# Performance work log

Measured on AMD Instinct MI355X. Metric: run time of the kernel, lower is better.

The kernel has to match this reference:

```python
import jax, jax.numpy as jnp
import numpy as np

LUT_DIM = 33
CTX_DIM = 128


def _identity_lut(dim):
    coords = jnp.linspace(0.0, 1.0, dim)
    r, g, b = jnp.meshgrid(coords, coords, coords, indexing='ij')
    return jnp.stack([r, g, b], axis=-1)  # [dim, dim, dim, 3], axes (r,g,b)


def setup_inputs() -> dict:
    key = jax.random.key(0)
    ks = jax.random.split(key, 8)
    B, H, W = 4, 512, 512
    image = jax.random.normal(ks[0], (B, 3, H, W), dtype=jnp.float32)
    spatial_context = jax.random.normal(ks[1], (B, CTX_DIM, H, W), dtype=jnp.float32)
    s = 0.05
    params = {
        'base_lut': _identity_lut(LUT_DIM),
        'W1': jax.random.normal(ks[2], (128, CTX_DIM), dtype=jnp.float32) * s,
        'b1': jnp.zeros((128,), dtype=jnp.float32),
        'W2': jax.random.normal(ks[3], (64, 128), dtype=jnp.float32) * s,
        'b2': jnp.zeros((64,), dtype=jnp.float32),
        'W3': jax.random.normal(ks[4], (3, 64), dtype=jnp.float32) * s,
        'b3': jnp.zeros((3,), dtype=jnp.float32),
        'offset_scale': jnp.float32(0.1),
    }
    return {'image': image, 'spatial_context': spatial_context, **params}


def _conv1x1(x, W, b):
    # x: [B,Cin,H,W], W: [Cout,Cin]
    return jnp.einsum('bchw,oc->bohw', x, W) + b[None, :, None, None]


def _trilinear_lut(lut_flat, gx, gy, gz, dim):
    # lut_flat: [3, dim^3] (flattened over z,y,x = r,g,b axes)
    # gx,gy,gz: [B,H,W] float coords in [0, dim-1]; border padding via clamp
    fmax = jnp.float32(dim - 1)
    gx = jnp.clip(gx, 0.0, fmax)
    gy = jnp.clip(gy, 0.0, fmax)
    gz = jnp.clip(gz, 0.0, fmax)
    x0 = jnp.floor(gx).astype(jnp.int32)
    y0 = jnp.floor(gy).astype(jnp.int32)
    z0 = jnp.floor(gz).astype(jnp.int32)
    x1 = jnp.minimum(x0 + 1, dim - 1)
    y1 = jnp.minimum(y0 + 1, dim - 1)
    z1 = jnp.minimum(z0 + 1, dim - 1)
    fx = gx - x0.astype(gx.dtype)
    fy = gy - y0.astype(gy.dtype)
    fz = gz - z0.astype(gz.dtype)

    def gather(zi, yi, xi):
        idx = (zi * dim + yi) * dim + xi  # [B,H,W]
        return lut_flat[:, idx]  # [3,B,H,W]

    c000 = gather(z0, y0, x0); c001 = gather(z0, y0, x1)
    c010 = gather(z0, y1, x0); c011 = gather(z0, y1, x1)
    c100 = gather(z1, y0, x0); c101 = gather(z1, y0, x1)
    c110 = gather(z1, y1, x0); c111 = gather(z1, y1, x1)

    fx = fx[None]; fy = fy[None]; fz = fz[None]
    c00 = c000 * (1 - fx) + c001 * fx
    c01 = c010 * (1 - fx) + c011 * fx
    c10 = c100 * (1 - fx) + c101 * fx
    c11 = c110 * (1 - fx) + c111 * fx
    c0 = c00 * (1 - fy) + c01 * fy
    c1 = c10 * (1 - fy) + c11 * fy
    out = c0 * (1 - fz) + c1 * fz  # [3,B,H,W]
    return jnp.transpose(out, (1, 0, 2, 3))  # [B,3,H,W]


def reference(image, spatial_context, base_lut, W1, b1, W2, b2, W3, b3, offset_scale):
    dim = base_lut.shape[0]
    gelu = lambda v: jax.nn.gelu(v, approximate=False)
    h = gelu(_conv1x1(spatial_context, W1, b1))
    h = gelu(_conv1x1(h, W2, b2))
    offset = jnp.tanh(_conv1x1(h, W3, b3)) * offset_scale  # [B,3,H,W]

    img01 = jnp.clip((image + 1.0) * 0.5, 0.0, 1.0)
    # grid_sample convention: grid channel0 (R)->x->last LUT axis (b),
    # channel1 (G)->y->g axis, channel2 (B)->z->r axis; align_corners=True.
    scale = jnp.float32(dim - 1)
    gx = img01[:, 0] * scale  # R -> b axis
    gy = img01[:, 1] * scale  # G -> g axis
    gz = img01[:, 2] * scale  # B -> r axis
    # base_lut [r,g,b,3] -> channels-first [3, r(=z), g(=y), b(=x)] -> flatten
    lut_flat = jnp.transpose(base_lut, (3, 0, 1, 2)).reshape(3, dim * dim * dim)
    sampled = _trilinear_lut(lut_flat, gx, gy, gz, dim)  # [B,3,H,W]
    return sampled * 2.0 - 1.0 + offset
```

## Files before the change

### kernel.cpp

```cpp
#include <hip/hip_runtime.h>
#include <stdint.h>

#define HW 262144
#define LDIM 33

typedef __bf16 bf16x8 __attribute__((ext_vector_type(8)));
typedef float  f32x4  __attribute__((ext_vector_type(4)));

union BF8 { bf16x8 v; unsigned u[4]; };

__device__ __forceinline__ unsigned bfr1(float a) {
  unsigned u = __float_as_uint(a);
  return (u + 0x7fffu + ((u >> 16) & 1u)) >> 16;
}
__device__ __forceinline__ unsigned pk2(float a, float b) {
  return bfr1(a) | (bfr1(b) << 16);
}
__device__ __forceinline__ float tanh_fast(float x) {
  return 1.0f - 2.0f / (__expf(2.0f * x) + 1.0f);
}
__device__ __forceinline__ float gelu_t(float x) {
  float t = tanh_fast(0.7978845608028654f * (x + 0.044715f * x * x * x));
  return 0.5f * x * (1.0f + t);
}

__global__ __launch_bounds__(256, 2) void local3dlut_kernel(
    const float* __restrict__ img,  const float* __restrict__ ctx,
    const float* __restrict__ lut,  const float* __restrict__ W1,
    const float* __restrict__ b1,   const float* __restrict__ W2,
    const float* __restrict__ b2,   const float* __restrict__ W3,
    const float* __restrict__ b3,   const float* __restrict__ oscp,
    float* __restrict__ out)
{
  __shared__ uint4 smem4[4096];
  char* sm = (char*)smem4;
  const int t    = threadIdx.x;
  const int lane = t & 63;
  const int wv   = t >> 6;
  const int n    = lane & 15;
  const int q    = lane >> 4;

  #pragma unroll
  for (int rep = 0; rep < 16; ++rep) {
    int f4 = t + 256 * rep;
    float4 v = ((const float4*)W1)[f4];
    int fi = f4 << 2;
    int o = fi >> 7, k = fi & 127;
    char* dst = sm + o * 256 + (((k >> 3) ^ (o & 15)) << 4) + ((k & 7) << 1);
    *(uint2*)dst = make_uint2(pk2(v.x, v.y), pk2(v.z, v.w));
  }
  #pragma unroll
  for (int rep = 0; rep < 8; ++rep) {
    int f4 = t + 256 * rep;
    float4 v = ((const float4*)W2)[f4];
    int fi = f4 << 2;
    int o = fi >> 7, k = fi & 127;
    char* dst = sm + 32768 + o * 256 + (((k >> 3) ^ (o & 15)) << 4) + ((k & 7) << 1);
    *(uint2*)dst = make_uint2(pk2(v.x, v.y), pk2(v.z, v.w));
  }
  __syncthreads();

  float b1r[8], b2r[4], w3r[3][4];
  #pragma unroll
  for (int i = 0; i < 8; ++i) b1r[i] = b1[i * 16 + n];
  #pragma unroll
  for (int i = 0; i < 4; ++i) b2r[i] = b2[i * 16 + n];
  #pragma unroll
  for (int j = 0; j < 3; ++j)
    #pragma unroll
    for (int i = 0; i < 4; ++i) w3r[j][i] = W3[j * 64 + i * 16 + n];
  const float b3r0 = b3[0], b3r1 = b3[1], b3r2 = b3[2];
  const float osc  = oscp[0];

  const int p0   = blockIdx.x * 512;
  const int bi   = p0 >> 18;
  const int sblk = p0 & (HW - 1);
  const float* ctxB = ctx + (size_t)bi * ((size_t)128 * HW);
  const float* imgB = img + (size_t)bi * ((size_t)3 * HW);
  float*       outB = out + (size_t)bi * ((size_t)3 * HW);
  char* hb = sm + 49152 + wv * 4096;

  #pragma unroll 1
  for (int it = 0; it < 4; ++it) {
    const int sw = sblk + it * 128 + wv * 32;

    BF8 a1[2][4];
    #pragma unroll
    for (int mt = 0; mt < 2; ++mt) {
      const int sA = sw + mt * 16 + n;
      #pragma unroll
      for (int ks = 0; ks < 4; ++ks) {
        const float* cb = ctxB + (size_t)(ks * 32 + q * 8) * HW + sA;
        float v0 = cb[0];
        float v1 = cb[(size_t)1 * HW];
        float v2 = cb[(size_t)2 * HW];
        float v3 = cb[(size_t)3 * HW];
        float v4 = cb[(size_t)4 * HW];
        float v5 = cb[(size_t)5 * HW];
        float v6 = cb[(size_t)6 * HW];
        float v7 = cb[(size_t)7 * HW];
        a1[mt][ks].u[0] = pk2(v0, v1);
        a1[mt][ks].u[1] = pk2(v2, v3);
        a1[mt][ks].u[2] = pk2(v4, v5);
        a1[mt][ks].u[3] = pk2(v6, v7);
      }
    }

    f32x4 acc2[2][4];
    #pragma unroll
    for (int mt = 0; mt < 2; ++mt)
      #pragma unroll
      for (int j = 0; j < 4; ++j) { f32x4 z = {0.f,0.f,0.f,0.f}; acc2[mt][j] = z; }

    #pragma unroll
    for (int half = 0; half < 2; ++half) {
      f32x4 acc1[2][4];
      #pragma unroll
      for (int mt = 0; mt < 2; ++mt)
        #pragma unroll
        for (int j = 0; j < 4; ++j) { f32x4 z = {0.f,0.f,0.f,0.f}; acc1[mt][j] = z; }

      #pragma unroll
      for (int ks = 0; ks < 4; ++ks) {
        #pragma unroll
        for (int nt4 = 0; nt4 < 4; ++nt4) {
          int row = (half * 4 + nt4) * 16 + n;
          bf16x8 bw = *(const bf16x8*)(sm + row * 256 + ((((ks << 2) + q) ^ n) << 4));
          acc1[0][nt4] = __builtin_amdgcn_mfma_f32_16x16x32_bf16(a1[0][ks].v, bw, acc1[0][nt4], 0, 0, 0);
          acc1[1][nt4] = __builtin_amdgcn_mfma_f32_16x16x32_bf16(a1[1][ks].v, bw, acc1[1][nt4], 0, 0, 0);
        }
      }
      #pragma unroll
      for (int mt = 0; mt < 2; ++mt)
        #pragma unroll
        for (int nt4 = 0; nt4 < 4; ++nt4) {
          int fl = nt4 * 16 + n;
          int kgf = fl >> 3;
          #pragma unroll
          for (int r = 0; r < 4; ++r) {
            int px = mt * 16 + (q << 2) + r;
            float hv = gelu_t(acc1[mt][nt4][r] + b1r[half * 4 + nt4]);
            *(unsigned short*)(hb + px * 128 + ((kgf ^ (px & 7)) << 4) + ((fl & 7) << 1)) =
                (unsigned short)bfr1(hv);
          }
        }
      #pragma unroll
      for (int ks2 = 0; ks2 < 2; ++ks2) {
        bf16x8 a2[2];
        #pragma unroll
        for (int mt = 0; mt < 2; ++mt) {
          int px = mt * 16 + n;
          a2[mt] = *(const bf16x8*)(hb + px * 128 + ((((ks2 << 2) + q) ^ (px & 7)) << 4));
        }
        #pragma unroll
        for (int nt2 = 0; nt2 < 4; ++nt2) {
          int row = nt2 * 16 + n;
          int kg2 = half * 8 + (ks2 << 2) + q;
          bf16x8 bw = *(const bf16x8*)(sm + 32768 + row * 256 + ((kg2 ^ n) << 4));
          acc2[0][nt2] = __builtin_amdgcn_mfma_f32_16x16x32_bf16(a2[0], bw, acc2[0][nt2], 0, 0, 0);
          acc2[1][nt2] = __builtin_amdgcn_mfma_f32_16x16x32_bf16(a2[1], bw, acc2[1][nt2], 0, 0, 0);
        }
      }
    }

    #pragma unroll
    for (int mt = 0; mt < 2; ++mt)
      #pragma unroll
      for (int nt2 = 0; nt2 < 4; ++nt2)
        #pragma unroll
        for (int r = 0; r < 4; ++r)
          acc2[mt][nt2][r] = gelu_t(acc2[mt][nt2][r] + b2r[nt2]);

    #pragma unroll
    for (int mt = 0; mt < 2; ++mt)
      #pragma unroll
      for (int r = 0; r < 4; ++r) {
        float h0 = acc2[mt][0][r], h1v = acc2[mt][1][r], h2v = acc2[mt][2][r], h3v = acc2[mt][3][r];
        float pa = w3r[0][0]*h0 + w3r[0][1]*h1v + w3r[0][2]*h2v + w3r[0][3]*h3v;
        float pb = w3r[1][0]*h0 + w3r[1][1]*h1v + w3r[1][2]*h2v + w3r[1][3]*h3v;
        float pc = w3r[2][0]*h0 + w3r[2][1]*h1v + w3r[2][2]*h2v + w3r[2][3]*h3v;
        pa += __shfl_xor(pa, 1, 16); pa += __shfl_xor(pa, 2, 16);
        pa += __shfl_xor(pa, 4, 16); pa += __shfl_xor(pa, 8, 16);
        pb += __shfl_xor(pb, 1, 16); pb += __shfl_xor(pb, 2, 16);
        pb += __shfl_xor(pb, 4, 16); pb += __shfl_xor(pb, 8, 16);
        pc += __shfl_xor(pc, 1, 16); pc += __shfl_xor(pc, 2, 16);
        pc += __shfl_xor(pc, 4, 16); pc += __shfl_xor(pc, 8, 16);
        int px = mt * 16 + (q << 2) + r;
        float sel  = (n == 0) ? pa   : ((n == 1) ? pb   : pc);
        float bsel = (n == 0) ? b3r0 : ((n == 1) ? b3r1 : b3r2);
        float ov = tanh_fast(sel + bsel) * osc;
        if (n < 3) *(float*)(hb + px * 12 + (n << 2)) = ov;
      }

    if (lane < 32) {
      const int sp = sw + lane;
      float o0 = *(const float*)(hb + lane * 12 + 0);
      float o1 = *(const float*)(hb + lane * 12 + 4);
      float o2 = *(const float*)(hb + lane * 12 + 8);

      float rr = imgB[sp], gg = imgB[HW + sp], bb = imgB[2 * HW + sp];
      float gx = fminf(fmaxf((rr + 1.f) * 0.5f, 0.f), 1.f) * 32.f;
      float gy = fminf(fmaxf((gg + 1.f) * 0.5f, 0.f), 1.f) * 32.f;
      float gz = fminf(fmaxf((bb + 1.f) * 0.5f, 0.f), 1.f) * 32.f;
      int x0 = (int)gx, y0 = (int)gy, z0 = (int)gz;
      float fx = gx - (float)x0, fy = gy - (float)y0, fz = gz - (float)z0;
      int x1 = min(x0 + 1, 32), y1 = min(y0 + 1, 32), z1 = min(z0 + 1, 32);
      int zy00 = (z0 * LDIM + y0) * LDIM, zy01 = (z0 * LDIM + y1) * LDIM;
      int zy10 = (z1 * LDIM + y0) * LDIM, zy11 = (z1 * LDIM + y1) * LDIM;
      int i000 = (zy00 + x0) * 3, i001 = (zy00 + x1) * 3;
      int i010 = (zy01 + x0) * 3, i011 = (zy01 + x1) * 3;
      int i100 = (zy10 + x0) * 3, i101 = (zy10 + x1) * 3;
      int i110 = (zy11 + x0) * 3, i111 = (zy11 + x1) * 3;
      const float* L = lut;
      float so[3];
      #pragma unroll
      for (int ch = 0; ch < 3; ++ch) {
        float c000 = L[i000 + ch], c001 = L[i001 + ch];
        float c010 = L[i010 + ch], c011 = L[i011 + ch];
        float c100 = L[i100 + ch], c101 = L[i101 + ch];
        float c110 = L[i110 + ch], c111 = L[i111 + ch];
        float c00 = c000 + fx * (c001 - c000);
        float c01 = c010 + fx * (c011 - c010);
        float c10 = c100 + fx * (c101 - c100);
        float c11 = c110 + fx * (c111 - c110);
        float ca  = c00 + fy * (c01 - c00);
        float cb2 = c10 + fy * (c11 - c10);
        so[ch] = ca + fz * (cb2 - ca);
      }
      outB[sp]          = so[0] * 2.f - 1.f + o0;
      outB[HW + sp]     = so[1] * 2.f - 1.f + o1;
      outB[2 * HW + sp] = so[2] * 2.f - 1.f + o2;
    }
  }
}

extern "C" void kernel_launch(void* const* d_in, const int* in_sizes, int n_in,
                              void* d_out, int out_size, void* d_ws, size_t ws_size,
                              hipStream_t stream) {
  const float* img = (const float*)d_in[0];
  const float* ctx = (const float*)d_in[1];
  const float* lut = (const float*)d_in[2];
  const float* W1  = (const float*)d_in[3];
  const float* b1  = (const float*)d_in[4];
  const float* W2  = (const float*)d_in[5];
  const float* b2  = (const float*)d_in[6];
  const float* W3  = (const float*)d_in[7];
  const float* b3  = (const float*)d_in[8];
  const float* osc = (const float*)d_in[9];
  float* out = (float*)d_out;
  local3dlut_kernel<<<dim3(2048), dim3(256), 0, stream>>>(
      img, ctx, lut, W1, b1, W2, b2, W3, b3, osc, out);
}
```

Baseline: 828.1 us.

## Transpose second MFMA output, simplify GELU math, and parallelize LUT stage across lanes

```diff
diff --git a/kernel.cpp b/kernel.cpp
--- a/kernel.cpp
+++ b/kernel.cpp
@@ -5,23 +5,23 @@
 #define LDIM 33
 
 typedef __bf16 bf16x8 __attribute__((ext_vector_type(8)));
+typedef __bf16 bf16x2 __attribute__((ext_vector_type(2)));
 typedef float  f32x4  __attribute__((ext_vector_type(4)));
 
 union BF8 { bf16x8 v; unsigned u[4]; };
 
-__device__ __forceinline__ unsigned bfr1(float a) {
-  unsigned u = __float_as_uint(a);
-  return (u + 0x7fffu + ((u >> 16) & 1u)) >> 16;
-}
 __device__ __forceinline__ unsigned pk2(float a, float b) {
-  return bfr1(a) | (bfr1(b) << 16);
+  bf16x2 p; p[0] = (__bf16)a; p[1] = (__bf16)b;
+  return __builtin_bit_cast(unsigned, p);
 }
 __device__ __forceinline__ float tanh_fast(float x) {
-  return 1.0f - 2.0f / (__expf(2.0f * x) + 1.0f);
+  return 1.0f - __fdividef(2.0f, __expf(2.0f * x) + 1.0f);
 }
 __device__ __forceinline__ float gelu_t(float x) {
-  float t = tanh_fast(0.7978845608028654f * (x + 0.044715f * x * x * x));
-  return 0.5f * x * (1.0f + t);
+  float x2 = x * x;
+  float p  = x * fmaf(0.0713548163f, x2, 1.5957691216f);
+  float r  = __fdividef(1.0f, __expf(p) + 1.0f);
+  return fmaf(-x, r, x);
 }
 
 __global__ __launch_bounds__(256, 2) void local3dlut_kernel(
@@ -60,16 +60,22 @@
   }
   __syncthreads();
 
-  float b1r[8], b2r[4], w3r[3][4];
+  float b1r[8];
   #pragma unroll
   for (int i = 0; i < 8; ++i) b1r[i] = b1[i * 16 + n];
-  #pragma unroll
-  for (int i = 0; i < 4; ++i) b2r[i] = b2[i * 16 + n];
-  #pragma unroll
-  for (int j = 0; j < 3; ++j)
-    #pragma unroll
-    for (int i = 0; i < 4; ++i) w3r[j][i] = W3[j * 64 + i * 16 + n];
-  const float b3r0 = b3[0], b3r1 = b3[1], b3r2 = b3[2];
+  float b2l[4][4];
+  #pragma unroll
+  for (int i = 0; i < 4; ++i)
+    #pragma unroll
+    for (int r = 0; r < 4; ++r) b2l[i][r] = b2[i * 16 + (q << 2) + r];
+  float w3l[3][4][4];
+  #pragma unroll
+  for (int c = 0; c < 3; ++c)
+    #pragma unroll
+    for (int i = 0; i < 4; ++i)
+      #pragma unroll
+      for (int r = 0; r < 4; ++r) w3l[c][i][r] = W3[c * 64 + i * 16 + (q << 2) + r];
+  const float b3a0 = b3[0], b3a1 = b3[1], b3a2 = b3[2];
   const float osc  = oscp[0];
 
   const int p0   = blockIdx.x * 512;
@@ -83,6 +89,13 @@
   #pragma unroll 1
   for (int it = 0; it < 4; ++it) {
     const int sw = sblk + it * 128 + wv * 32;
+
+    const float ri0 = imgB[sw + n];
+    const float gi0 = imgB[HW + sw + n];
+    const float bi0 = imgB[2 * HW + sw + n];
+    const float ri1 = imgB[sw + 16 + n];
+    const float gi1 = imgB[HW + sw + 16 + n];
+    const float bi1 = imgB[2 * HW + sw + 16 + n];
 
     BF8 a1[2][4];
     #pragma unroll
@@ -140,8 +153,7 @@
           for (int r = 0; r < 4; ++r) {
             int px = mt * 16 + (q << 2) + r;
             float hv = gelu_t(acc1[mt][nt4][r] + b1r[half * 4 + nt4]);
-            *(unsigned short*)(hb + px * 128 + ((kgf ^ (px & 7)) << 4) + ((fl & 7) << 1)) =
-                (unsigned short)bfr1(hv);
+            *(__bf16*)(hb + px * 128 + ((kgf ^ (px & 7)) << 4) + ((fl & 7) << 1)) = (__bf16)hv;
           }
         }
       #pragma unroll
@@ -157,8 +169,8 @@
           int row = nt2 * 16 + n;
           int kg2 = half * 8 + (ks2 << 2) + q;
           bf16x8 bw = *(const bf16x8*)(sm + 32768 + row * 256 + ((kg2 ^ n) << 4));
-          acc2[0][nt2] = __builtin_amdgcn_mfma_f32_16x16x32_bf16(a2[0], bw, acc2[0][nt2], 0, 0, 0);
-          acc2[1][nt2] = __builtin_amdgcn_mfma_f32_16x16x32_bf16(a2[1], bw, acc2[1][nt2], 0, 0, 0);
+          acc2[0][nt2] = __builtin_amdgcn_mfma_f32_16x16x32_bf16(bw, a2[0], acc2[0][nt2], 0, 0, 0);
+          acc2[1][nt2] = __builtin_amdgcn_mfma_f32_16x16x32_bf16(bw, a2[1], acc2[1][nt2], 0, 0, 0);
         }
       }
     }
@@ -169,67 +181,58 @@
       for (int nt2 = 0; nt2 < 4; ++nt2)
         #pragma unroll
         for (int r = 0; r < 4; ++r)
-          acc2[mt][nt2][r] = gelu_t(acc2[mt][nt2][r] + b2r[nt2]);
-
-    #pragma unroll
-    for (int mt = 0; mt < 2; ++mt)
-      #pragma unroll
-      for (int r = 0; r < 4; ++r) {
-        float h0 = acc2[mt][0][r], h1v = acc2[mt][1][r], h2v = acc2[mt][2][r], h3v = acc2[mt][3][r];
-        float pa = w3r[0][0]*h0 + w3r[0][1]*h1v + w3r[0][2]*h2v + w3r[0][3]*h3v;
-        float pb = w3r[1][0]*h0 + w3r[1][1]*h1v + w3r[1][2]*h2v + w3r[1][3]*h3v;
-        float pc = w3r[2][0]*h0 + w3r[2][1]*h1v + w3r[2][2]*h2v + w3r[2][3]*h3v;
-        pa += __shfl_xor(pa, 1, 16); pa += __shfl_xor(pa, 2, 16);
-        pa += __shfl_xor(pa, 4, 16); pa += __shfl_xor(pa, 8, 16);
-        pb += __shfl_xor(pb, 1, 16); pb += __shfl_xor(pb, 2, 16);
-        pb += __shfl_xor(pb, 4, 16); pb += __shfl_xor(pb, 8, 16);
-        pc += __shfl_xor(pc, 1, 16); pc += __shfl_xor(pc, 2, 16);
-        pc += __shfl_xor(pc, 4, 16); pc += __shfl_xor(pc, 8, 16);
-        int px = mt * 16 + (q << 2) + r;
-        float sel  = (n == 0) ? pa   : ((n == 1) ? pb   : pc);
-        float bsel = (n == 0) ? b3r0 : ((n == 1) ? b3r1 : b3r2);
-        float ov = tanh_fast(sel + bsel) * osc;
-        if (n < 3) *(float*)(hb + px * 12 + (n << 2)) = ov;
-      }
-
-    if (lane < 32) {
-      const int sp = sw + lane;
-      float o0 = *(const float*)(hb + lane * 12 + 0);
-      float o1 = *(const float*)(hb + lane * 12 + 4);
-      float o2 = *(const float*)(hb + lane * 12 + 8);
-
-      float rr = imgB[sp], gg = imgB[HW + sp], bb = imgB[2 * HW + sp];
-      float gx = fminf(fmaxf((rr + 1.f) * 0.5f, 0.f), 1.f) * 32.f;
-      float gy = fminf(fmaxf((gg + 1.f) * 0.5f, 0.f), 1.f) * 32.f;
-      float gz = fminf(fmaxf((bb + 1.f) * 0.5f, 0.f), 1.f) * 32.f;
-      int x0 = (int)gx, y0 = (int)gy, z0 = (int)gz;
-      float fx = gx - (float)x0, fy = gy - (float)y0, fz = gz - (float)z0;
-      int x1 = min(x0 + 1, 32), y1 = min(y0 + 1, 32), z1 = min(z0 + 1, 32);
-      int zy00 = (z0 * LDIM + y0) * LDIM, zy01 = (z0 * LDIM + y1) * LDIM;
-      int zy10 = (z1 * LDIM + y0) * LDIM, zy11 = (z1 * LDIM + y1) * LDIM;
-      int i000 = (zy00 + x0) * 3, i001 = (zy00 + x1) * 3;
-      int i010 = (zy01 + x0) * 3, i011 = (zy01 + x1) * 3;
-      int i100 = (zy10 + x0) * 3, i101 = (zy10 + x1) * 3;
-      int i110 = (zy11 + x0) * 3, i111 = (zy11 + x1) * 3;
+          acc2[mt][nt2][r] = gelu_t(acc2[mt][nt2][r] + b2l[nt2][r]);
+
+    float o0[3], o1[3];
+    #pragma unroll
+    for (int ch = 0; ch < 3; ++ch) {
+      float s0 = 0.f, s1 = 0.f;
+      #pragma unroll
+      for (int nt2 = 0; nt2 < 4; ++nt2)
+        #pragma unroll
+        for (int r = 0; r < 4; ++r) {
+          s0 = fmaf(w3l[ch][nt2][r], acc2[0][nt2][r], s0);
+          s1 = fmaf(w3l[ch][nt2][r], acc2[1][nt2][r], s1);
+        }
+      s0 += __shfl_xor(s0, 16); s0 += __shfl_xor(s0, 32);
+      s1 += __shfl_xor(s1, 16); s1 += __shfl_xor(s1, 32);
+      float bch = (ch == 0) ? b3a0 : ((ch == 1) ? b3a1 : b3a2);
+      o0[ch] = tanh_fast(s0 + bch) * osc;
+      o1[ch] = tanh_fast(s1 + bch) * osc;
+    }
+
+    if (q < 3) {
+      const float ov0 = (q == 0) ? o0[0] : ((q == 1) ? o0[1] : o0[2]);
+      const float ov1 = (q == 0) ? o1[0] : ((q == 1) ? o1[1] : o1[2]);
       const float* L = lut;
-      float so[3];
-      #pragma unroll
-      for (int ch = 0; ch < 3; ++ch) {
-        float c000 = L[i000 + ch], c001 = L[i001 + ch];
-        float c010 = L[i010 + ch], c011 = L[i011 + ch];
-        float c100 = L[i100 + ch], c101 = L[i101 + ch];
-        float c110 = L[i110 + ch], c111 = L[i111 + ch];
+      #pragma unroll
+      for (int mt = 0; mt < 2; ++mt) {
+        const float rr = mt ? ri1 : ri0;
+        const float gg = mt ? gi1 : gi0;
+        const float bb = mt ? bi1 : bi0;
+        const float ov = mt ? ov1 : ov0;
+        const int sp = sw + mt * 16 + n;
+        float gx = fminf(fmaxf((rr + 1.f) * 0.5f, 0.f), 1.f) * 32.f;
+        float gy = fminf(fmaxf((gg + 1.f) * 0.5f, 0.f), 1.f) * 32.f;
+        float gz = fminf(fmaxf((bb + 1.f) * 0.5f, 0.f), 1.f) * 32.f;
+        int x0 = (int)gx, y0 = (int)gy, z0 = (int)gz;
+        float fx = gx - (float)x0, fy = gy - (float)y0, fz = gz - (float)z0;
+        int x1 = min(x0 + 1, 32), y1 = min(y0 + 1, 32), z1 = min(z0 + 1, 32);
+        int zy00 = (z0 * LDIM + y0) * LDIM, zy01 = (z0 * LDIM + y1) * LDIM;
+        int zy10 = (z1 * LDIM + y0) * LDIM, zy11 = (z1 * LDIM + y1) * LDIM;
+        float c000 = L[(zy00 + x0) * 3 + q], c001 = L[(zy00 + x1) * 3 + q];
+        float c010 = L[(zy01 + x0) * 3 + q], c011 = L[(zy01 + x1) * 3 + q];
+        float c100 = L[(zy10 + x0) * 3 + q], c101 = L[(zy10 + x1) * 3 + q];
+        float c110 = L[(zy11 + x0) * 3 + q], c111 = L[(zy11 + x1) * 3 + q];
         float c00 = c000 + fx * (c001 - c000);
         float c01 = c010 + fx * (c011 - c010);
         float c10 = c100 + fx * (c101 - c100);
         float c11 = c110 + fx * (c111 - c110);
         float ca  = c00 + fy * (c01 - c00);
         float cb2 = c10 + fy * (c11 - c10);
-        so[ch] = ca + fz * (cb2 - ca);
-      }
-      outB[sp]          = so[0] * 2.f - 1.f + o0;
-      outB[HW + sp]     = so[1] * 2.f - 1.f + o1;
-      outB[2 * HW + sp] = so[2] * 2.f - 1.f + o2;
+        float so  = ca + fz * (cb2 - ca);
+        outB[q * HW + sp] = so * 2.f - 1.f + ov;
+      }
     }
   }
 }
```

After: 788.3 us. -4.8%, faster.
